# Kernel tuning notes

Measured on AMD Instinct MI355X. Metric: run time of the kernel, lower is better.

The kernel has to match this reference:

```python
import jax, jax.numpy as jnp
import numpy as np

N = 50000
E = 1600000
EPS = 1e-16


def transformer_conv(x, src, dst, ea, Wq, bq, Wk, bk, Wv, bv, We, Ws, bs):
    # PyG TransformerConv, heads=1, concat=True, root_weight=True
    C = Wq.shape[1]
    q = x @ Wq + bq                      # [N, C]
    k = x @ Wk + bk                      # [N, C]
    v = x @ Wv + bv                      # [N, C]
    e = ea @ We                          # [E, C]
    k_e = k[src] + e                     # per-edge key
    v_e = v[src] + e                     # per-edge value
    score = (q[dst] * k_e).sum(-1) / jnp.sqrt(jnp.asarray(C, x.dtype))  # [E]
    # segment softmax over incoming edges of each dst node
    m = jax.ops.segment_max(score, dst, num_segments=N)
    ex = jnp.exp(score - m[dst])
    denom = jax.ops.segment_sum(ex, dst, num_segments=N)
    alpha = ex / (denom[dst] + EPS)
    out = jax.ops.segment_sum(alpha[:, None] * v_e, dst, num_segments=N)
    return out + x @ Ws + bs             # skip connection


def gcn_conv(x, src, dst, W, b):
    # PyG GCNConv: self-loops + symmetric deg^-1/2 normalization
    n_idx = jnp.arange(N)
    src2 = jnp.concatenate([src, n_idx])
    dst2 = jnp.concatenate([dst, n_idx])
    deg = jax.ops.segment_sum(jnp.ones(E + N, x.dtype), dst2, num_segments=N)
    dinv = jnp.where(deg > 0, jax.lax.rsqrt(deg), 0.0)
    norm = dinv[src2] * dinv[dst2]       # [E+N]
    h = x @ W                            # [N, out]
    out = jax.ops.segment_sum(norm[:, None] * h[src2], dst2, num_segments=N)
    return out + b


def setup_inputs() -> dict:
    key = jax.random.key(0)
    ks = jax.random.split(key, 32)
    d = {}
    d['x'] = jax.random.normal(ks[0], (N, 128), jnp.float32)
    d['edge_index'] = jax.random.randint(ks[1], (2, E), 0, N, jnp.int64)
    d['edge_attr'] = jax.random.normal(ks[2], (E, 16), jnp.float32)
    shapes = dict(
        Wq1=(128, 96), bq1=(96,), Wk1=(128, 96), bk1=(96,), Wv1=(128, 96), bv1=(96,),
        We1=(16, 96), Ws1=(128, 96), bs1=(96,),
        Wq2=(96, 64), bq2=(64,), Wk2=(96, 64), bk2=(64,), Wv2=(96, 64), bv2=(64,),
        We2=(16, 64), Ws2=(96, 64), bs2=(64,),
        Wmu=(64, 32), bmu=(32,), Wls=(64, 32), bls=(32,))
    for i, (name, shp) in enumerate(shapes.items()):
        scale = 1.0 / np.sqrt(shp[0]) if len(shp) == 2 else 0.02
        d[name] = jax.random.normal(ks[3 + i], shp, jnp.float32) * scale
    return d


def reference(x, edge_index, edge_attr,
              Wq1, bq1, Wk1, bk1, Wv1, bv1, We1, Ws1, bs1,
              Wq2, bq2, Wk2, bk2, Wv2, bv2, We2, Ws2, bs2,
              Wmu, bmu, Wls, bls):
    src, dst = edge_index[0], edge_index[1]
    h = jax.nn.relu(transformer_conv(x, src, dst, edge_attr,
                                     Wq1, bq1, Wk1, bk1, Wv1, bv1, We1, Ws1, bs1))
    h = jax.nn.relu(transformer_conv(h, src, dst, edge_attr,
                                     Wq2, bq2, Wk2, bk2, Wv2, bv2, We2, Ws2, bs2))
    mu = gcn_conv(h, src, dst, Wmu, bmu)
    logstd = gcn_conv(h, src, dst, Wls, bls)
    return mu, logstd
```

## Files before the change

### kernel.cpp

```cpp
#include <hip/hip_runtime.h>
#include <math.h>


#define TPB 256
typedef unsigned int uint32;
typedef unsigned long long u64;
typedef unsigned short u16;
typedef __attribute__((ext_vector_type(4))) float f32x4;
typedef __attribute__((ext_vector_type(4))) uint32 u32x4;
typedef __attribute__((ext_vector_type(8))) short bf16x8;

__device__ __forceinline__ uint32 f2bf(float f) {
    uint32 u = __float_as_uint(f);
    return (u + 0x7fffu + ((u >> 16) & 1u)) >> 16;
}
__device__ __forceinline__ float bf2f(uint32 b) { return __uint_as_float(b << 16); }

__global__ void hist_kernel(const int* __restrict__ dst, int* __restrict__ deg, int E) {
    int i = blockIdx.x * TPB + threadIdx.x;
    if (i < E) atomicAdd(&deg[__builtin_nontemporal_load(dst + i)], 1);
}

__global__ __launch_bounds__(1024) void scan1_kernel(const int* __restrict__ deg,
                                                     int* __restrict__ prowp,
                                                     int* __restrict__ bsum, int n) {
    __shared__ int wsum[16];
    __shared__ int woff[16];
    int tid = threadIdx.x;
    int i = blockIdx.x * 1024 + tid;
    int lane = tid & 63, w = tid >> 6;
    int dg = (i < n) ? deg[i] : 0;
    int x = (dg + 7) & ~7;
    int v = x;
#pragma unroll
    for (int off = 1; off < 64; off <<= 1) {
        int t = __shfl_up(v, off, 64);
        if (lane >= off) v += t;
    }
    if (lane == 63) wsum[w] = v;
    __syncthreads();
    if (tid < 64) {
        int s = (tid < 16) ? wsum[tid] : 0;
#pragma unroll
        for (int off = 1; off < 16; off <<= 1) {
            int t = __shfl_up(s, off, 64);
            if (lane >= off) s += t;
        }
        if (tid < 16) woff[tid] = s;
    }
    __syncthreads();
    int incl = v + (w ? woff[w - 1] : 0);
    if (i < n) prowp[i] = incl;
    if (tid == 1023) bsum[blockIdx.x] = incl;
}

__global__ void scan2_kernel(const int* __restrict__ bsum, int* __restrict__ boff,
                             int* __restrict__ prowpN, int nb) {
    int tid = threadIdx.x;
    int x = (tid < nb) ? bsum[tid] : 0;
    int v = x;
#pragma unroll
    for (int off = 1; off < 64; off <<= 1) {
        int t = __shfl_up(v, off, 64);
        if (tid >= off) v += t;
    }
    if (tid < nb) boff[tid] = v - x;
    if (tid == nb - 1) *prowpN = v;
}

__global__ __launch_bounds__(1024) void scan3_kernel(const int* __restrict__ deg,
                                                     const int* __restrict__ boff,
                                                     int* __restrict__ prowp,
                                                     int* __restrict__ cursor,
                                                     float* __restrict__ dinv, int n) {
    int i = blockIdx.x * 1024 + threadIdx.x;
    if (i < n) {
        int dg = deg[i];
        int x = (dg + 7) & ~7;
        int excl = prowp[i] - x + boff[blockIdx.x];
        prowp[i] = excl;
        cursor[i] = excl;
        dinv[i] = 1.0f / sqrtf((float)(dg + 1));
    }
}

__global__ void scatter_kernel(const int* __restrict__ src, const int* __restrict__ dst,
                               const float* __restrict__ EA,
                               int* __restrict__ cursor,
                               u64* __restrict__ pse, u16* __restrict__ EAbE, int E) {
    int i = blockIdx.x * TPB + threadIdx.x;
    if (i >= E) return;
    int s = __builtin_nontemporal_load(src + i);
    int d0 = __builtin_nontemporal_load(dst + i);
    int pos = atomicAdd(&cursor[d0], 1);
    pse[pos] = ((u64)(uint32)i << 32) | (uint32)s;
    const f32x4* e4 = (const f32x4*)(EA + (size_t)i * 16);
    f32x4 a = __builtin_nontemporal_load(e4);
    f32x4 b = __builtin_nontemporal_load(e4 + 1);
    f32x4 c = __builtin_nontemporal_load(e4 + 2);
    f32x4 d = __builtin_nontemporal_load(e4 + 3);
    u32x4 lo = {f2bf(a.x) | (f2bf(a.y) << 16), f2bf(a.z) | (f2bf(a.w) << 16),
                f2bf(b.x) | (f2bf(b.y) << 16), f2bf(b.z) | (f2bf(b.w) << 16)};
    u32x4 hi = {f2bf(c.x) | (f2bf(c.y) << 16), f2bf(c.z) | (f2bf(c.w) << 16),
                f2bf(d.x) | (f2bf(d.y) << 16), f2bf(d.z) | (f2bf(d.w) << 16)};
    u32x4* o = (u32x4*)(EAbE + (size_t)i * 16);
    __builtin_nontemporal_store(lo, o);
    __builtin_nontemporal_store(hi, o + 1);
}

__global__ void padfill_kernel(const int* __restrict__ prowp, const int* __restrict__ deg,
                               u64* __restrict__ pse, int N, int E) {
    int n = blockIdx.x * TPB + threadIdx.x;
    if (n >= N) return;
    int p = prowp[n] + deg[n], pe = prowp[n + 1];
    u64 pad = ((u64)(uint32)E << 32) | (uint32)N;
    for (; p < pe; ++p) pse[p] = pad;
}

__global__ void zerorow_kernel(u16* __restrict__ EAbE, int E) {
    if (threadIdx.x < 16) EAbE[(size_t)E * 16 + threadIdx.x] = 0;
}

__global__ void pack_kernel(
    const float* Wq1, const float* Wk1, const float* Wv1, const float* Ws1,
    const float* bq1, const float* bk1, const float* bv1, const float* bs1,
    const float* We1,
    const float* Wq2, const float* Wk2, const float* Wv2, const float* Ws2,
    const float* bq2, const float* bk2, const float* bv2, const float* bs2,
    const float* We2,
    const float* Wmu, const float* bmu, const float* Wls, const float* bls,
    const float* x, unsigned short* xb, int NX,
    unsigned short* Wc1t, float* bc1, unsigned short* Wc2t, float* bc2,
    float* Wc3, float* bc3) {
    const float s1 = 0.1020620726159658f;
    const float s2 = 0.125f;
    int gi = blockIdx.x * TPB + threadIdx.x;
    const int R0 = 448 * 128, R1 = R0 + 320 * 96, R2 = R1 + 64 * 64;
    const int R3 = R2 + 448, R4 = R3 + 320, R5 = R4 + 64;
    for (int i = gi; i < R5; i += gridDim.x * TPB) {
        if (i < R0) {
            int c = i / 128, kk = i % 128;
            float v = 0.f;
            if (c < 96) v = Wq1[kk * 96 + c] * s1;
            else if (c < 112) {
                int t = c - 96; float a = 0.f;
                for (int u = 0; u < 96; ++u) a += Wq1[kk * 96 + u] * We1[t * 96 + u];
                v = a * s1;
            } else if (c < 304) {
                int tt = c - 112;
                v = (tt & 1) ? Wv1[kk * 96 + (tt >> 1)] : Wk1[kk * 96 + (tt >> 1)];
            } else if (c < 400) v = Ws1[kk * 96 + (c - 304)];
            Wc1t[i] = (unsigned short)f2bf(v);
        } else if (i < R1) {
            int j = i - R0;
            int c = j / 96, kk = j % 96;
            float v = 0.f;
            if (c < 64) v = Wq2[kk * 64 + c] * s2;
            else if (c < 80) {
                int t = c - 64; float a = 0.f;
                for (int u = 0; u < 64; ++u) a += Wq2[kk * 64 + u] * We2[t * 64 + u];
                v = a * s2;
            } else if (c < 208) {
                int tt = c - 80;
                v = (tt & 1) ? Wv2[kk * 64 + (tt >> 1)] : Wk2[kk * 64 + (tt >> 1)];
            } else if (c < 272) v = Ws2[kk * 64 + (c - 208)];
            Wc2t[j] = (unsigned short)f2bf(v);
        } else if (i < R2) {
            int j = i - R1;
            int k = j / 64, c = j % 64;
            Wc3[j] = (c < 32) ? Wmu[k * 32 + c] : Wls[k * 32 + (c - 32)];
        } else if (i < R3) {
            int c = i - R2;
            float v = 0.f;
            if (c < 96) v = bq1[c] * s1;
            else if (c < 112) {
                int t = c - 96; float a = 0.f;
                for (int u = 0; u < 96; ++u) a += bq1[u] * We1[t * 96 + u];
                v = a * s1;
            } else if (c < 304) {
                int tt = c - 112;
                v = (tt & 1) ? bv1[tt >> 1] : bk1[tt >> 1];
            } else if (c < 400) v = bs1[c - 304];
            bc1[c] = v;
        } else if (i < R4) {
            int c = i - R3;
            float v = 0.f;
            if (c < 64) v = bq2[c] * s2;
            else if (c < 80) {
                int t = c - 64; float a = 0.f;
                for (int u = 0; u < 64; ++u) a += bq2[u] * We2[t * 64 + u];
                v = a * s2;
            } else if (c < 208) {
                int tt = c - 80;
                v = (tt & 1) ? bv2[tt >> 1] : bk2[tt >> 1];
            } else if (c < 272) v = bs2[c - 208];
            bc2[c] = v;
        } else {
            int c = i - R4;
            bc3[c] = (c < 32) ? bmu[c] : bls[c - 32];
        }
    }
    for (int i = gi; i < NX; i += gridDim.x * TPB)
        xb[i] = (unsigned short)f2bf(x[i]);
}

__global__ __launch_bounds__(256) void mfma_gemm_kernel(
    const unsigned short* __restrict__ A,
    const unsigned short* __restrict__ Wt,
    const float* __restrict__ bias,
    float* __restrict__ Qs, float* __restrict__ QE,
    uint32* __restrict__ KVp, float* __restrict__ SK,
    int N, int K, int Cq) {
    __shared__ unsigned short As[64][56];
    __shared__ unsigned short Bs[64][56];
    int r0 = blockIdx.x * 64, c0 = blockIdx.y * 64;
    int tid = threadIdx.x;
    int lane = tid & 63, w = tid >> 6;
    int wm = w >> 1, wn = w & 1;
    int l15 = lane & 15, l4 = lane >> 4;
    f32x4 zero = {0.f, 0.f, 0.f, 0.f};
    f32x4 acc[2][2] = {{zero, zero}, {zero, zero}};
    int sr = tid >> 2, sk = (tid & 3) * 8;

    for (int kc = 0; kc < K; kc += 32) {
        bf16x8 av = {};
        int ar = r0 + sr;
        if (ar < N) av = *(const bf16x8*)(A + (size_t)ar * K + kc + sk);
        *(bf16x8*)&As[sr][sk] = av;
        bf16x8 bv = *(const bf16x8*)(Wt + (size_t)(c0 + sr) * K + kc + sk);
        *(bf16x8*)&Bs[sr][sk] = bv;
        __syncthreads();
        bf16x8 af0 = *(const bf16x8*)&As[32 * wm + l15][l4 * 8];
        bf16x8 af1 = *(const bf16x8*)&As[32 * wm + 16 + l15][l4 * 8];
        bf16x8 bf0 = *(const bf16x8*)&Bs[32 * wn + l15][l4 * 8];
        bf16x8 bf1 = *(const bf16x8*)&Bs[32 * wn + 16 + l15][l4 * 8];
        acc[0][0] = __builtin_amdgcn_mfma_f32_16x16x32_bf16(af0, bf0, acc[0][0], 0, 0, 0);
        acc[0][1] = __builtin_amdgcn_mfma_f32_16x16x32_bf16(af0, bf1, acc[0][1], 0, 0, 0);
        acc[1][0] = __builtin_amdgcn_mfma_f32_16x16x32_bf16(af1, bf0, acc[1][0], 0, 0, 0);
        acc[1][1] = __builtin_amdgcn_mfma_f32_16x16x32_bf16(af1, bf1, acc[1][1], 0, 0, 0);
        __syncthreads();
    }

    int qe0 = Cq, kv0 = Cq + 16, sk0 = 3 * Cq + 16, end0 = 4 * Cq + 16;
#pragma unroll
    for (int fm = 0; fm < 2; ++fm) {
#pragma unroll
        for (int fn = 0; fn < 2; ++fn) {
            int cb = c0 + 32 * wn + 16 * fn;
            int c = cb + l15;
            float bia = bias[c];
#pragma unroll
            for (int r = 0; r < 4; ++r) {
                int row = r0 + 32 * wm + 16 * fm + l4 * 4 + r;
                float v = acc[fm][fn][r] + bia;
                float pv = __shfl_xor(v, 1, 64);
                bool ok = row < N;
                if (cb < qe0) {
                    if (ok) Qs[(size_t)row * Cq + c] = v;
                } else if (cb < kv0) {
                    if (ok) QE[(size_t)row * 16 + (c - qe0)] = v;
                } else if (cb < sk0) {
                    if (ok && !(l15 & 1)) {
                        int t = c - kv0;
                        KVp[(size_t)row * Cq + (t >> 1)] = (f2bf(v) << 16) | f2bf(pv);
                    }
                } else if (cb < end0) {
                    if (ok) SK[(size_t)row * Cq + (c - sk0)] = v;
                }
            }
        }
    }
}

template <int C>
__global__ __launch_bounds__(256) void edge_attn_kernel(
    const float* __restrict__ Qs, const float* __restrict__ SK,
    const uint32* __restrict__ KVp,
    const u16* __restrict__ EAbE, const float* __restrict__ QE,
    const int* __restrict__ prowp, const int* __restrict__ deg,
    const u64* __restrict__ pse,
    float* __restrict__ Hpre, float* __restrict__ AEA, int N) {
    constexpr int CPL = C / 32;
    int n = blockIdx.x * 4 + (threadIdx.x >> 6);
    if (n >= N) return;
    int lane = threadIdx.x & 63;
    int half = lane >> 5, l = lane & 31, t16 = l & 15;
    bool lo16 = (l < 16);

    uint32 nC = (uint32)n * C;
    float q[CPL], acc[CPL];
#pragma unroll
    for (int j = 0; j < CPL; ++j) { q[j] = Qs[nC + l + 32 * j]; acc[j] = 0.f; }
    float qe = lo16 ? QE[(uint32)n * 16 + t16] : 0.f;
    float d = 0.f, aea = 0.f;
    int eb = prowp[n], ee = prowp[n + 1];

    for (int base = eb + 8 * half; base < ee; base += 16) {
        const u64* pp = pse + base;
        float dots[8], eav[8];
        uint32 kv[8][CPL];
#pragma unroll
        for (int u = 0; u < 8; ++u) {
            u64 pk = __builtin_nontemporal_load(pp + u);
            uint32 s = (uint32)pk;
            uint32 eid = (uint32)(pk >> 32);
            eav[u] = bf2f((uint32)EAbE[(size_t)eid * 16 + t16]);
            uint32 off = s * C + l;
            float dt = qe * eav[u];
#pragma unroll
            for (int j = 0; j < CPL; ++j) {
                uint32 t = KVp[off + 32 * j];
                kv[u][j] = t;
                dt = fmaf(q[j], __uint_as_float(t & 0xffff0000u), dt);
            }
            dots[u] = dt;
        }
#pragma unroll
        for (int a = 0; a < 4; ++a) {
            float x0 = dots[2 * a], x1 = dots[2 * a + 1];
            float z = (lo16 ? x0 : x1) + __shfl_xor(lo16 ? x1 : x0, 16, 64);
            z += __shfl_xor(z, 8, 64);
            z += __shfl_xor(z, 4, 64);
            z += __shfl_xor(z, 2, 64);
            z += __shfl_xor(z, 1, 64);
            float p = __expf(z);
            float p0 = __shfl(p, 0, 32);
            float p1 = __shfl(p, 16, 32);
            d += p0 + p1;
            aea = fmaf(p0, eav[2 * a], fmaf(p1, eav[2 * a + 1], aea));
#pragma unroll
            for (int j = 0; j < CPL; ++j)
                acc[j] = fmaf(p0, __uint_as_float(kv[2 * a][j] << 16),
                         fmaf(p1, __uint_as_float(kv[2 * a + 1][j] << 16), acc[j]));
        }
    }
    d += __shfl_xor(d, 32, 64);
    aea += __shfl_xor(aea, 32, 64);
    d -= (float)((ee - eb) - deg[n]);
    float inv = 1.f / (d + 1e-16f);
#pragma unroll
    for (int j = 0; j < CPL; ++j) {
        float a2 = acc[j] + __shfl_xor(acc[j], 32, 64);
        if (half == 0)
            Hpre[nC + l + 32 * j] = a2 * inv + SK[nC + l + 32 * j];
    }
    if (lane < 16) AEA[(uint32)n * 16 + t16] = aea * inv;
}

template <int C>
__global__ void fixup_relu_kernel(const float* __restrict__ Hpre, const float* __restrict__ AEA,
                                  const float* __restrict__ We,
                                  unsigned short* __restrict__ H1b, int NC) {
    int idx = blockIdx.x * TPB + threadIdx.x;
    if (idx >= NC) return;
    int n = idx / C, c = idx % C;
    const float* a = AEA + (size_t)n * 16;
    float s = Hpre[idx];
#pragma unroll
    for (int t = 0; t < 16; ++t) s += a[t] * We[t * C + c];
    H1b[idx] = (unsigned short)f2bf(fmaxf(s, 0.f));
}

__global__ void fixup2_kernel(const float* __restrict__ Hpre, const float* __restrict__ AEA,
                              const float* __restrict__ We, const float* __restrict__ dinv,
                              uint32* __restrict__ H2p, int N) {
    int idx = blockIdx.x * TPB + threadIdx.x;
    if (idx >= N * 32) return;
    int n = idx >> 5, c = idx & 31;
    const float* a = AEA + (size_t)n * 16;
    float s0 = Hpre[(size_t)n * 64 + c];
    float s1 = Hpre[(size_t)n * 64 + 32 + c];
#pragma unroll
    for (int t = 0; t < 16; ++t) {
        s0 += a[t] * We[t * 64 + c];
        s1 += a[t] * We[t * 64 + 32 + c];
    }
    float dn = dinv[n];
    s0 = fmaxf(s0, 0.f) * dn;
    s1 = fmaxf(s1, 0.f) * dn;
    H2p[idx] = f2bf(s0) | (f2bf(s1) << 16);
}

__global__ __launch_bounds__(256) void gcn_agg_kernel(
    const uint32* __restrict__ H2p, const int* __restrict__ prowp,
    const u64* __restrict__ pse, const float* __restrict__ dinv,
    float* __restrict__ AGG, int N) {
    int n = blockIdx.x * 4 + (threadIdx.x >> 6);
    if (n >= N) return;
    int lane = threadIdx.x & 63, half = lane >> 5, l = lane & 31;
    float s0 = 0.f, s1 = 0.f;
    int eb = prowp[n], ee = prowp[n + 1];
    for (int base = eb + 8 * half; base < ee; base += 16) {
        const u64* pp = pse + base;
#pragma unroll
        for (int u = 0; u < 8; ++u) {
            uint32 s = (uint32)__builtin_nontemporal_load(pp + u);
            uint32 t = H2p[s * 32 + l];
            s0 += bf2f(t & 0xffffu);
            s1 += __uint_as_float(t & 0xffff0000u);
        }
    }
    s0 += __shfl_xor(s0, 32, 64);
    s1 += __shfl_xor(s1, 32, 64);
    if (half == 0) {
        uint32 u = H2p[(uint32)n * 32 + l];
        float dn = dinv[n];
        AGG[(uint32)n * 64 + l]      = dn * (s0 + bf2f(u & 0xffffu));
        AGG[(uint32)n * 64 + 32 + l] = dn * (s1 + __uint_as_float(u & 0xffff0000u));
    }
}

template <int CT, bool SPLIT>
__global__ __launch_bounds__(256) void gemm_kernel(
    const float* __restrict__ A, const float* __restrict__ W,
    const float* __restrict__ bias, float* __restrict__ Out,
    float* __restrict__ Out2, int N, int K, int C) {
    constexpr int TC = CT / 16;
    __shared__ float As[32][68];
    __shared__ float Bs[32][CT + 4];
    int r0 = blockIdx.x * 64, c0 = blockIdx.y * CT;
    int t = threadIdx.x;
    int tr = t >> 4, tc = t & 15;
    float acc[4][TC];
#pragma unroll
    for (int i = 0; i < 4; ++i)
#pragma unroll
        for (int j = 0; j < TC; ++j) acc[i][j] = 0.f;

    for (int kc = 0; kc < K; kc += 32) {
        int ra = t >> 2, kq = (t & 3) * 8;
        float4 a0 = {0, 0, 0, 0}, a1 = {0, 0, 0, 0};
        int r = r0 + ra;
        if (r < N) {
            const float* ap = A + (size_t)r * K + kc + kq;
            a0 = *(const float4*)ap;
            a1 = *(const float4*)(ap + 4);
        }
        As[kq + 0][ra] = a0.x; As[kq + 1][ra] = a0.y;
        As[kq + 2][ra] = a0.z; As[kq + 3][ra] = a0.w;
        As[kq + 4][ra] = a1.x; As[kq + 5][ra] = a1.y;
        As[kq + 6][ra] = a1.z; As[kq + 7][ra] = a1.w;
        constexpr int PASSES = (32 * CT) / (256 * 8);
#pragma unroll
        for (int p = 0; p < PASSES; ++p) {
            int idx = (t + p * 256) * 8;
            int k = idx / CT, c = idx % CT;
            const float* wp = W + (size_t)(kc + k) * C + c0 + c;
            float4 b0 = *(const float4*)wp;
            float4 b1 = *(const float4*)(wp + 4);
            *(float4*)&Bs[k][c] = b0;
            *(float4*)&Bs[k][c + 4] = b1;
        }
        __syncthreads();
#pragma unroll
        for (int k = 0; k < 32; ++k) {
            float4 av = *(const float4*)&As[k][tr * 4];
            float a[4] = {av.x, av.y, av.z, av.w};
#pragma unroll
            for (int u = 0; u < TC / 4; ++u) {
                float4 bv = *(const float4*)&Bs[k][tc * TC + u * 4];
                float b[4] = {bv.x, bv.y, bv.z, bv.w};
#pragma unroll
                for (int i = 0; i < 4; ++i)
#pragma unroll
                    for (int j = 0; j < 4; ++j) acc[i][u * 4 + j] += a[i] * b[j];
            }
        }
        __syncthreads();
    }
#pragma unroll
    for (int i = 0; i < 4; ++i) {
        int r = r0 + tr * 4 + i;
        if (r >= N) continue;
#pragma unroll
        for (int j = 0; j < TC; ++j) {
            int c = c0 + tc * TC + j;
            float v = acc[i][j] + bias[c];
            if (SPLIT) {
                if (c < 32) Out[(size_t)r * 32 + c] = v;
                else        Out2[(size_t)r * 32 + c - 32] = v;
            } else {
                Out[(size_t)r * C + c] = v;
            }
        }
    }
}

extern "C" void kernel_launch(void* const* d_in, const int* in_sizes, int n_in,
                              void* d_out, int out_size, void* d_ws, size_t ws_size,
                              hipStream_t stream) {
    const float* x   = (const float*)d_in[0];
    const int*   ei  = (const int*)d_in[1];
    const float* ea  = (const float*)d_in[2];
    const float* Wq1 = (const float*)d_in[3];  const float* bq1 = (const float*)d_in[4];
    const float* Wk1 = (const float*)d_in[5];  const float* bk1 = (const float*)d_in[6];
    const float* Wv1 = (const float*)d_in[7];  const float* bv1 = (const float*)d_in[8];
    const float* We1 = (const float*)d_in[9];
    const float* Ws1 = (const float*)d_in[10]; const float* bs1 = (const float*)d_in[11];
    const float* Wq2 = (const float*)d_in[12]; const float* bq2 = (const float*)d_in[13];
    const float* Wk2 = (const float*)d_in[14]; const float* bk2 = (const float*)d_in[15];
    const float* Wv2 = (const float*)d_in[16]; const float* bv2 = (const float*)d_in[17];
    const float* We2 = (const float*)d_in[18];
    const float* Ws2 = (const float*)d_in[19]; const float* bs2 = (const float*)d_in[20];
    const float* Wmu = (const float*)d_in[21]; const float* bmu = (const float*)d_in[22];
    const float* Wls = (const float*)d_in[23]; const float* bls = (const float*)d_in[24];

    int N = in_sizes[0] / 128;
    int E = in_sizes[1] / 2;
    const int* src = ei;
    const int* dst = ei + E;
    int E2max = E + 8 * N;

    char* ws = (char*)d_ws;
    size_t off = 0;
    auto alloc = [&](size_t bytes) -> char* {
        char* p = ws + off;
        off = (off + bytes + 255) & ~(size_t)255;
        return p;
    };
    int*      deg    = (int*)alloc((size_t)N * 4);
    int*      prowp  = (int*)alloc((size_t)(N + 1) * 4);
    int*      cursor = (int*)alloc((size_t)N * 4);
    float*    dinv   = (float*)alloc((size_t)N * 4);
    int*      bsum   = (int*)alloc(256 * 4);
    int*      boff   = (int*)alloc(256 * 4);
    u64*      pse    = (u64*)alloc((size_t)E2max * 8);
    u16*      EAbE   = (u16*)alloc((size_t)(E + 1) * 16 * 2);
    unsigned short* Wc1t = (unsigned short*)alloc(448 * 128 * 2);
    float*    bc1    = (float*)alloc(448 * 4);
    unsigned short* Wc2t = (unsigned short*)alloc(320 * 96 * 2);
    float*    bc2    = (float*)alloc(320 * 4);
    float*    Wc3    = (float*)alloc(64 * 64 * 4);
    float*    bc3    = (float*)alloc(64 * 4);
    unsigned short* xb = (unsigned short*)alloc((size_t)N * 128 * 2);
    float*    Qs   = (float*)alloc((size_t)N * 96 * 4);
    float*    QE   = (float*)alloc((size_t)N * 16 * 4);
    uint32*   KVp  = (uint32*)alloc((size_t)(N + 1) * 96 * 4);
    float*    SKb  = (float*)alloc((size_t)N * 96 * 4);
    float*    Hpre = (float*)alloc((size_t)N * 96 * 4);
    unsigned short* H1b = (unsigned short*)alloc((size_t)N * 96 * 2);
    float*    AEA  = (float*)alloc((size_t)N * 16 * 4);
    uint32*   H2p  = (uint32*)alloc((size_t)(N + 1) * 32 * 4);
    float*    AGG  = (float*)alloc((size_t)N * 64 * 4);

    (void)hipMemsetAsync(deg, 0, (size_t)N * 4, stream);
    (void)hipMemsetAsync(KVp + (size_t)N * 96, 0, 96 * 4, stream);
    (void)hipMemsetAsync(H2p + (size_t)N * 32, 0, 32 * 4, stream);

    int ebk = (E + TPB - 1) / TPB;
    int nb1k = (N + 1023) / 1024;
    int nbN = (N + TPB - 1) / TPB;
    hist_kernel<<<ebk, TPB, 0, stream>>>(dst, deg, E);
    scan1_kernel<<<nb1k, 1024, 0, stream>>>(deg, prowp, bsum, N);
    scan2_kernel<<<1, 64, 0, stream>>>(bsum, boff, prowp + N, nb1k);
    scan3_kernel<<<nb1k, 1024, 0, stream>>>(deg, boff, prowp, cursor, dinv, N);
    scatter_kernel<<<ebk, TPB, 0, stream>>>(src, dst, ea, cursor, pse, EAbE, E);
    padfill_kernel<<<nbN, TPB, 0, stream>>>(prowp, deg, pse, N, E);
    zerorow_kernel<<<1, 64, 0, stream>>>(EAbE, E);
    pack_kernel<<<364, TPB, 0, stream>>>(Wq1, Wk1, Wv1, Ws1, bq1, bk1, bv1, bs1, We1,
                                         Wq2, Wk2, Wv2, Ws2, bq2, bk2, bv2, bs2, We2,
                                         Wmu, bmu, Wls, bls, x, xb, N * 128,
                                         Wc1t, bc1, Wc2t, bc2, Wc3, bc3);

    int rb = (N + 63) / 64;
    int nb4 = (N + 3) / 4;

    mfma_gemm_kernel<<<dim3(rb, 7), 256, 0, stream>>>(xb, Wc1t, bc1, Qs, QE, KVp, SKb,
                                                      N, 128, 96);
    edge_attn_kernel<96><<<nb4, 256, 0, stream>>>(Qs, SKb, KVp, EAbE, QE, prowp, deg, pse,
                                                  Hpre, AEA, N);
    fixup_relu_kernel<96><<<(N * 96 + TPB - 1) / TPB, TPB, 0, stream>>>(Hpre, AEA, We1,
                                                                        H1b, N * 96);
    mfma_gemm_kernel<<<dim3(rb, 5), 256, 0, stream>>>(H1b, Wc2t, bc2, Qs, QE, KVp, SKb,
                                                      N, 96, 64);
    (void)hipMemsetAsync(KVp + (size_t)N * 64, 0, 64 * 4, stream);
    edge_attn_kernel<64><<<nb4, 256, 0, stream>>>(Qs, SKb, KVp, EAbE, QE, prowp, deg, pse,
                                                  Hpre, AEA, N);
    fixup2_kernel<<<(N * 32 + TPB - 1) / TPB, TPB, 0, stream>>>(Hpre, AEA, We2, dinv, H2p, N);
    gcn_agg_kernel<<<nb4, 256, 0, stream>>>(H2p, prowp, pse, dinv, AGG, N);
    gemm_kernel<64, true><<<dim3(rb, 1), 256, 0, stream>>>(AGG, Wc3, bc3, (float*)d_out,
                                                           (float*)d_out + (size_t)N * 32,
                                                           N, 64, 64);
}
```

Baseline: 536.2 us.

## Drop bf16 edge-attr copy, fuse padfill into scan, prefetch edge indices

Removes the preprocessing pass that converted edge attributes to bf16, and has the attention kernels gather fp32 edge attributes directly, masking padded edges by source index. Padding writes move into the scan kernel, which removes two small launches. The attention loop now prefetches the next batch of packed edge indices and issues all gathers before the dot products. In exchange, each attention pass reads twice as many edge-attribute bytes.

Result: slower. 580.5 us (+8.3%).

```diff
diff --git a/kernel.cpp b/kernel.cpp
--- a/kernel.cpp
+++ b/kernel.cpp
@@ -7,7 +7,6 @@
 typedef unsigned long long u64;
 typedef unsigned short u16;
 typedef __attribute__((ext_vector_type(4))) float f32x4;
-typedef __attribute__((ext_vector_type(4))) uint32 u32x4;
 typedef __attribute__((ext_vector_type(8))) short bf16x8;
 
 __device__ __forceinline__ uint32 f2bf(float f) {
@@ -72,7 +71,8 @@
                                                      const int* __restrict__ boff,
                                                      int* __restrict__ prowp,
                                                      int* __restrict__ cursor,
-                                                     float* __restrict__ dinv, int n) {
+                                                     float* __restrict__ dinv,
+                                                     u64* __restrict__ pse, int n) {
     int i = blockIdx.x * 1024 + threadIdx.x;
     if (i < n) {
         int dg = deg[i];
@@ -81,44 +81,19 @@
         prowp[i] = excl;
         cursor[i] = excl;
         dinv[i] = 1.0f / sqrtf((float)(dg + 1));
+        u64 pad = (u64)(uint32)n;
+        for (int p = excl + dg; p < excl + x; ++p) pse[p] = pad;
     }
 }
 
 __global__ void scatter_kernel(const int* __restrict__ src, const int* __restrict__ dst,
-                               const float* __restrict__ EA,
-                               int* __restrict__ cursor,
-                               u64* __restrict__ pse, u16* __restrict__ EAbE, int E) {
+                               int* __restrict__ cursor, u64* __restrict__ pse, int E) {
     int i = blockIdx.x * TPB + threadIdx.x;
     if (i >= E) return;
     int s = __builtin_nontemporal_load(src + i);
     int d0 = __builtin_nontemporal_load(dst + i);
     int pos = atomicAdd(&cursor[d0], 1);
     pse[pos] = ((u64)(uint32)i << 32) | (uint32)s;
-    const f32x4* e4 = (const f32x4*)(EA + (size_t)i * 16);
-    f32x4 a = __builtin_nontemporal_load(e4);
-    f32x4 b = __builtin_nontemporal_load(e4 + 1);
-    f32x4 c = __builtin_nontemporal_load(e4 + 2);
-    f32x4 d = __builtin_nontemporal_load(e4 + 3);
-    u32x4 lo = {f2bf(a.x) | (f2bf(a.y) << 16), f2bf(a.z) | (f2bf(a.w) << 16),
-                f2bf(b.x) | (f2bf(b.y) << 16), f2bf(b.z) | (f2bf(b.w) << 16)};
-    u32x4 hi = {f2bf(c.x) | (f2bf(c.y) << 16), f2bf(c.z) | (f2bf(c.w) << 16),
-                f2bf(d.x) | (f2bf(d.y) << 16), f2bf(d.z) | (f2bf(d.w) << 16)};
-    u32x4* o = (u32x4*)(EAbE + (size_t)i * 16);
-    __builtin_nontemporal_store(lo, o);
-    __builtin_nontemporal_store(hi, o + 1);
-}
-
-__global__ void padfill_kernel(const int* __restrict__ prowp, const int* __restrict__ deg,
-                               u64* __restrict__ pse, int N, int E) {
-    int n = blockIdx.x * TPB + threadIdx.x;
-    if (n >= N) return;
-    int p = prowp[n] + deg[n], pe = prowp[n + 1];
-    u64 pad = ((u64)(uint32)E << 32) | (uint32)N;
-    for (; p < pe; ++p) pse[p] = pad;
-}
-
-__global__ void zerorow_kernel(u16* __restrict__ EAbE, int E) {
-    if (threadIdx.x < 16) EAbE[(size_t)E * 16 + threadIdx.x] = 0;
 }
 
 __global__ void pack_kernel(
@@ -276,7 +251,7 @@
 __global__ __launch_bounds__(256) void edge_attn_kernel(
     const float* __restrict__ Qs, const float* __restrict__ SK,
     const uint32* __restrict__ KVp,
-    const u16* __restrict__ EAbE, const float* __restrict__ QE,
+    const float* __restrict__ EA, const float* __restrict__ QE,
     const int* __restrict__ prowp, const int* __restrict__ deg,
     const u64* __restrict__ pse,
     float* __restrict__ Hpre, float* __restrict__ AEA, int N) {
@@ -295,24 +270,41 @@
     float d = 0.f, aea = 0.f;
     int eb = prowp[n], ee = prowp[n + 1];
 
-    for (int base = eb + 8 * half; base < ee; base += 16) {
-        const u64* pp = pse + base;
+    int base = eb + 8 * half;
+    u64 pk[8];
+    if (base < ee) {
+#pragma unroll
+        for (int u = 0; u < 8; ++u) pk[u] = __builtin_nontemporal_load(pse + base + u);
+    }
+    while (base < ee) {
+        int nbase = base + 16;
+        bool more = nbase < ee;
+        u64 pkn[8];
+        if (more) {
+#pragma unroll
+            for (int u = 0; u < 8; ++u) pkn[u] = __builtin_nontemporal_load(pse + nbase + u);
+        }
+        float eaR[8];
+        uint32 sv[8];
+        uint32 kv[8][CPL];
+#pragma unroll
+        for (int u = 0; u < 8; ++u) {
+            uint32 s = (uint32)pk[u];
+            uint32 eid = (uint32)(pk[u] >> 32);
+            sv[u] = s;
+            eaR[u] = EA[(size_t)eid * 16 + t16];
+            uint32 off2 = s * C + l;
+#pragma unroll
+            for (int j = 0; j < CPL; ++j) kv[u][j] = KVp[off2 + 32 * j];
+        }
         float dots[8], eav[8];
-        uint32 kv[8][CPL];
 #pragma unroll
         for (int u = 0; u < 8; ++u) {
-            u64 pk = __builtin_nontemporal_load(pp + u);
-            uint32 s = (uint32)pk;
-            uint32 eid = (uint32)(pk >> 32);
-            eav[u] = bf2f((uint32)EAbE[(size_t)eid * 16 + t16]);
-            uint32 off = s * C + l;
+            eav[u] = (sv[u] == (uint32)N) ? 0.f : eaR[u];
             float dt = qe * eav[u];
 #pragma unroll
-            for (int j = 0; j < CPL; ++j) {
-                uint32 t = KVp[off + 32 * j];
-                kv[u][j] = t;
-                dt = fmaf(q[j], __uint_as_float(t & 0xffff0000u), dt);
-            }
+            for (int j = 0; j < CPL; ++j)
+                dt = fmaf(q[j], __uint_as_float(kv[u][j] & 0xffff0000u), dt);
             dots[u] = dt;
         }
 #pragma unroll
@@ -333,6 +325,9 @@
                 acc[j] = fmaf(p0, __uint_as_float(kv[2 * a][j] << 16),
                          fmaf(p1, __uint_as_float(kv[2 * a + 1][j] << 16), acc[j]));
         }
+#pragma unroll
+        for (int u = 0; u < 8; ++u) pk[u] = pkn[u];
+        base = nbase;
     }
     d += __shfl_xor(d, 32, 64);
     aea += __shfl_xor(aea, 32, 64);
@@ -525,7 +520,6 @@
     int*      bsum   = (int*)alloc(256 * 4);
     int*      boff   = (int*)alloc(256 * 4);
     u64*      pse    = (u64*)alloc((size_t)E2max * 8);
-    u16*      EAbE   = (u16*)alloc((size_t)(E + 1) * 16 * 2);
     unsigned short* Wc1t = (unsigned short*)alloc(448 * 128 * 2);
     float*    bc1    = (float*)alloc(448 * 4);
     unsigned short* Wc2t = (unsigned short*)alloc(320 * 96 * 2);
@@ -549,14 +543,11 @@
 
     int ebk = (E + TPB - 1) / TPB;
     int nb1k = (N + 1023) / 1024;
-    int nbN = (N + TPB - 1) / TPB;
     hist_kernel<<<ebk, TPB, 0, stream>>>(dst, deg, E);
     scan1_kernel<<<nb1k, 1024, 0, stream>>>(deg, prowp, bsum, N);
     scan2_kernel<<<1, 64, 0, stream>>>(bsum, boff, prowp + N, nb1k);
-    scan3_kernel<<<nb1k, 1024, 0, stream>>>(deg, boff, prowp, cursor, dinv, N);
-    scatter_kernel<<<ebk, TPB, 0, stream>>>(src, dst, ea, cursor, pse, EAbE, E);
-    padfill_kernel<<<nbN, TPB, 0, stream>>>(prowp, deg, pse, N, E);
-    zerorow_kernel<<<1, 64, 0, stream>>>(EAbE, E);
+    scan3_kernel<<<nb1k, 1024, 0, stream>>>(deg, boff, prowp, cursor, dinv, pse, N);
+    scatter_kernel<<<ebk, TPB, 0, stream>>>(src, dst, cursor, pse, E);
     pack_kernel<<<364, TPB, 0, stream>>>(Wq1, Wk1, Wv1, Ws1, bq1, bk1, bv1, bs1, We1,
                                          Wq2, Wk2, Wv2, Ws2, bq2, bk2, bv2, bs2, We2,
                                          Wmu, bmu, Wls, bls, x, xb, N * 128,
@@ -567,14 +558,14 @@
 
     mfma_gemm_kernel<<<dim3(rb, 7), 256, 0, stream>>>(xb, Wc1t, bc1, Qs, QE, KVp, SKb,
                                                       N, 128, 96);
-    edge_attn_kernel<96><<<nb4, 256, 0, stream>>>(Qs, SKb, KVp, EAbE, QE, prowp, deg, pse,
+    edge_attn_kernel<96><<<nb4, 256, 0, stream>>>(Qs, SKb, KVp, ea, QE, prowp, deg, pse,
                                                   Hpre, AEA, N);
     fixup_relu_kernel<96><<<(N * 96 + TPB - 1) / TPB, TPB, 0, stream>>>(Hpre, AEA, We1,
                                                                         H1b, N * 96);
     mfma_gemm_kernel<<<dim3(rb, 5), 256, 0, stream>>>(H1b, Wc2t, bc2, Qs, QE, KVp, SKb,
                                                       N, 96, 64);
     (void)hipMemsetAsync(KVp + (size_t)N * 64, 0, 64 * 4, stream);
-    edge_attn_kernel<64><<<nb4, 256, 0, stream>>>(Qs, SKb, KVp, EAbE, QE, prowp, deg, pse,
+    edge_attn_kernel<64><<<nb4, 256, 0, stream>>>(Qs, SKb, KVp, ea, QE, prowp, deg, pse,
                                                   Hpre, AEA, N);
     fixup2_kernel<<<(N * 32 + TPB - 1) / TPB, TPB, 0, stream>>>(Hpre, AEA, We2, dinv, H2p, N);
     gcn_agg_kernel<<<nb4, 256, 0, stream>>>(H2p, prowp, pse, dinv, AGG, N);
```
